# Kernel optimization log

Measured on AMD Instinct MI355X. Metric: run time of the kernel, lower is better.

Reference implementation:

```python
import jax, jax.numpy as jnp
import numpy as np

LONG, LAT = 256, 256
N = LONG * LAT
BATCH = 64
OUT_DIM = 16 * 16


def _build_coo():
    # Faithful reproduction of the torch init loops (vectorized):
    # identity diagonal + 8-neighbor stencil entries for interior rows,
    # each (x,y) pair added in BOTH (x,y) and (y,x) directions.
    # torch sparse matmul on the uncoalesced COO sums duplicate entries,
    # so shared interior edges effectively get weight 2 -- the .at[].add
    # scatter below reproduces exactly that summation semantics.
    diag = np.arange(N, dtype=np.int64)
    centers = np.arange(LAT + 1, (LONG - 1) * LAT - 1, dtype=np.int64)
    offs = np.array([-1, 1, LAT, -LAT, LAT - 1, LAT + 1, -LAT - 1, -LAT + 1], dtype=np.int64)
    neigh = (centers[:, None] + offs[None, :]).ravel()
    crep = np.repeat(centers, 8)
    rows = np.concatenate([diag, crep, neigh]).astype(np.int32)
    cols = np.concatenate([diag, neigh, crep]).astype(np.int32)
    vals = np.ones(rows.shape[0], dtype=np.float32)
    return rows, cols, vals


def setup_inputs() -> dict:
    key = jax.random.key(0)
    k1, k2, k3 = jax.random.split(key, 3)
    rows, cols, vals = _build_coo()
    x = jax.random.normal(k1, (BATCH, LONG, LAT), dtype=jnp.float32)
    W = jax.random.normal(k2, (OUT_DIM, N), dtype=jnp.float32) * 0.02  # lin1.weight
    b = jax.random.normal(k3, (OUT_DIM,), dtype=jnp.float32) * 0.02   # lin1.bias
    return {
        "x": x,
        "W": W,
        "b": b,
        "rows": jnp.asarray(rows),
        "cols": jnp.asarray(cols),
        "vals": jnp.asarray(vals),
    }


def reference(x, W, b, rows, cols, vals):
    B = x.shape[0]
    xf = x.reshape(B, -1)                      # [B, N]
    gathered = xf[:, cols] * vals               # [B, E]
    h1 = jnp.zeros((B, xf.shape[1]), xf.dtype).at[:, rows].add(gathered)  # A @ xf.T, transposed
    h2 = h1 @ W.T + b                           # dense linear
    return h2
```

## Files before the change

### kernel.cpp

```cpp
#include <hip/hip_runtime.h>
#include <hip/hip_bf16.h>


#define MB    64
#define NOUT  256
#define KDIM  65536
#define NTOT  (MB * KDIM)
#define KSP   256
#define NCH   (KDIM / KSP)
#define OTOT  (MB * NOUT)
#define LSTR  272

typedef __attribute__((ext_vector_type(8))) short bf16x8;
typedef __attribute__((ext_vector_type(8))) unsigned short ushort8v;
typedef __attribute__((ext_vector_type(4))) float f32x4;

__device__ __forceinline__ ushort f2bf(float f) {
    __hip_bfloat16 h = __float2bfloat16(f);
    return *reinterpret_cast<ushort*>(&h);
}
__device__ __forceinline__ float bf2f(ushort u) {
    return __uint_as_float((unsigned)u << 16);
}

__device__ __forceinline__ void stencil16v(const float* __restrict__ x, int g,
                                           ushort8v* o0, ushort8v* o1) {
    const int i8 = g & (KDIM - 1);
    union Span { float4 v[6]; float f[24]; };
    Span u, c, d;
    #pragma unroll
    for (int q = 0; q < 6; ++q) {
        int bu = g - 260 + 4 * q; if (bu < 0) bu = 0;
        int bc = g - 4   + 4 * q; if (bc < 0) bc = 0; if (bc > NTOT - 4) bc = NTOT - 4;
        int bd = g + 252 + 4 * q; if (bd > NTOT - 4) bd = NTOT - 4;
        u.v[q] = *(const float4*)(x + bu);
        c.v[q] = *(const float4*)(x + bc);
        d.v[q] = *(const float4*)(x + bd);
    }
    if (i8 >= 514 && i8 <= 65006) {
        #pragma unroll
        for (int e = 0; e < 16; ++e) {
            float nb = c.f[3 + e] + c.f[5 + e]
                     + u.f[3 + e] + u.f[4 + e] + u.f[5 + e]
                     + d.f[3 + e] + d.f[4 + e] + d.f[5 + e];
            const ushort o = f2bf(fmaf(2.0f, nb, c.f[4 + e]));
            if (e < 8) (*o0)[e] = o; else (*o1)[e - 8] = o;
        }
    } else {
        #pragma unroll
        for (int e = 0; e < 16; ++e) {
            const int ii = i8 + e;
            const float ci = ((unsigned)(ii - 257) <= (65278u - 257u)) ? 1.0f : 0.0f;
            float s = c.f[4 + e];
            const int   doff[8] = {-1, 1, -257, -256, -255, 255, 256, 257};
            const float* src[8] = {&c.f[3 + e], &c.f[5 + e],
                                   &u.f[3 + e], &u.f[4 + e], &u.f[5 + e],
                                   &d.f[3 + e], &d.f[4 + e], &d.f[5 + e]};
            #pragma unroll
            for (int t = 0; t < 8; ++t) {
                const int j = ii + doff[t];
                const float cj = ((unsigned)(j - 257) <= (65278u - 257u)) ? 1.0f : 0.0f;
                s = fmaf(ci + cj, *src[t], s);
            }
            const ushort o = f2bf(s);
            if (e < 8) (*o0)[e] = o; else (*o1)[e - 8] = o;
        }
    }
}

__global__ __launch_bounds__(1024, 4) void fused_sg(const float* __restrict__ x,
                                                    const float* __restrict__ W,
                                                    ushort* __restrict__ part) {
    __shared__ ushort hs[MB * LSTR];
    const int b  = blockIdx.x;
    const int kp = (b & 7) * 32 + (b >> 3);
    const int t  = threadIdx.x;

    {
        const int m = t >> 4;
        const int j = t & 15;
        const int g = m * KDIM + kp * KSP + j * 16;
        ushort8v o0, o1;
        stencil16v(x, g, &o0, &o1);
        *(ushort8v*)&hs[m * LSTR + j * 16]     = o0;
        *(ushort8v*)&hs[m * LSTR + j * 16 + 8] = o1;
    }
    __syncthreads();

    const int nt = t >> 6;
    const int l  = t & 63;
    const int lr = l & 15;
    const int lg = l >> 4;

    f32x4 acc0 = (f32x4){0.f,0.f,0.f,0.f}, acc1 = (f32x4){0.f,0.f,0.f,0.f};
    f32x4 acc2 = (f32x4){0.f,0.f,0.f,0.f}, acc3 = (f32x4){0.f,0.f,0.f,0.f};

    const float* wp = W + (size_t)(nt * 16 + lr) * KDIM + kp * KSP + lg * 8;

    #pragma unroll
    for (int ks = 0; ks < KSP / 32; ++ks) {
        float4 w0 = *(const float4*)(wp + ks * 32);
        float4 w1 = *(const float4*)(wp + ks * 32 + 4);
        union { ushort u[8]; bf16x8 v; } bb;
        bb.u[0] = f2bf(w0.x); bb.u[1] = f2bf(w0.y);
        bb.u[2] = f2bf(w0.z); bb.u[3] = f2bf(w0.w);
        bb.u[4] = f2bf(w1.x); bb.u[5] = f2bf(w1.y);
        bb.u[6] = f2bf(w1.z); bb.u[7] = f2bf(w1.w);
        bf16x8 af0 = *(const bf16x8*)&hs[(0 * 16 + lr) * LSTR + lg * 8 + ks * 32];
        bf16x8 af1 = *(const bf16x8*)&hs[(1 * 16 + lr) * LSTR + lg * 8 + ks * 32];
        bf16x8 af2 = *(const bf16x8*)&hs[(2 * 16 + lr) * LSTR + lg * 8 + ks * 32];
        bf16x8 af3 = *(const bf16x8*)&hs[(3 * 16 + lr) * LSTR + lg * 8 + ks * 32];
        acc0 = __builtin_amdgcn_mfma_f32_16x16x32_bf16(af0, bb.v, acc0, 0, 0, 0);
        acc1 = __builtin_amdgcn_mfma_f32_16x16x32_bf16(af1, bb.v, acc1, 0, 0, 0);
        acc2 = __builtin_amdgcn_mfma_f32_16x16x32_bf16(af2, bb.v, acc2, 0, 0, 0);
        acc3 = __builtin_amdgcn_mfma_f32_16x16x32_bf16(af3, bb.v, acc3, 0, 0, 0);
    }

    ushort* pb = part + (size_t)kp * OTOT + (size_t)(nt * 16 + lr) * MB;
    ushort4 s;
    s.x = f2bf(acc0[0]); s.y = f2bf(acc0[1]); s.z = f2bf(acc0[2]); s.w = f2bf(acc0[3]);
    *(ushort4*)(pb + 0 * 16 + lg * 4) = s;
    s.x = f2bf(acc1[0]); s.y = f2bf(acc1[1]); s.z = f2bf(acc1[2]); s.w = f2bf(acc1[3]);
    *(ushort4*)(pb + 1 * 16 + lg * 4) = s;
    s.x = f2bf(acc2[0]); s.y = f2bf(acc2[1]); s.z = f2bf(acc2[2]); s.w = f2bf(acc2[3]);
    *(ushort4*)(pb + 2 * 16 + lg * 4) = s;
    s.x = f2bf(acc3[0]); s.y = f2bf(acc3[1]); s.z = f2bf(acc3[2]); s.w = f2bf(acc3[3]);
    *(ushort4*)(pb + 3 * 16 + lg * 4) = s;
}

__global__ __launch_bounds__(256) void reduce_bf16(const ushort* __restrict__ part,
                                                   const float* __restrict__ bias,
                                                   float* __restrict__ out) {
    __shared__ float red[256];
    const int ol = threadIdx.x & 15;
    const int cg = threadIdx.x >> 4;
    const int o  = blockIdx.x * 16 + ol;
    const ushort* p = part + (size_t)cg * 16 * OTOT + o;
    float s0 = 0.f, s1 = 0.f, s2 = 0.f, s3 = 0.f;
    #pragma unroll
    for (int i = 0; i < 16; i += 4) {
        s0 += bf2f(p[(size_t)(i + 0) * OTOT]);
        s1 += bf2f(p[(size_t)(i + 1) * OTOT]);
        s2 += bf2f(p[(size_t)(i + 2) * OTOT]);
        s3 += bf2f(p[(size_t)(i + 3) * OTOT]);
    }
    red[threadIdx.x] = (s0 + s1) + (s2 + s3);
    __syncthreads();
    if (cg == 0) {
        float v = red[ol];
        #pragma unroll
        for (int jj = 1; jj < 16; ++jj) v += red[jj * 16 + ol];
        const int n = o >> 6, m = o & 63;
        out[m * NOUT + n] = v + bias[n];
    }
}

extern "C" void kernel_launch(void* const* d_in, const int* in_sizes, int n_in,
                              void* d_out, int out_size, void* d_ws, size_t ws_size,
                              hipStream_t stream) {
    const float* x    = (const float*)d_in[0];
    const float* W    = (const float*)d_in[1];
    const float* bias = (const float*)d_in[2];
    float* out = (float*)d_out;

    ushort* part = (ushort*)d_ws;

    fused_sg<<<NCH, 1024, 0, stream>>>(x, W, part);
    reduce_bf16<<<OTOT / 16, 256, 0, stream>>>(part, bias, out);
}
```

Baseline: 35.05 us.

## Use 2D 16x16 spatial tiles with shared-memory staged stencil halo

Each block now covers a 16x16 spatial tile instead of one 256-wide row strip. It first loads the tile plus a one-cell halo for all 64 batches into shared memory as bf16, then computes the 9-point stencil from shared memory. This is meant to stop each thread from re-reading three overlapping rows straight from global memory. The cost is a larger shared-memory footprint, which may lower occupancy, an extra sync, and W loads that are now strided across rows. The input is also rounded to bf16 before the stencil sums, which adds rounding error.

Result: no change. 35.69 us (+1.8%).

```diff
diff --git a/kernel.cpp b/kernel.cpp
--- a/kernel.cpp
+++ b/kernel.cpp
@@ -6,10 +6,10 @@
 #define NOUT  256
 #define KDIM  65536
 #define NTOT  (MB * KDIM)
-#define KSP   256
-#define NCH   (KDIM / KSP)
 #define OTOT  (MB * NOUT)
 #define LSTR  272
+#define XSM   432
+#define XSR   24
 
 typedef __attribute__((ext_vector_type(8))) short bf16x8;
 typedef __attribute__((ext_vector_type(8))) unsigned short ushort8v;
@@ -23,67 +23,82 @@
     return __uint_as_float((unsigned)u << 16);
 }
 
-__device__ __forceinline__ void stencil16v(const float* __restrict__ x, int g,
-                                           ushort8v* o0, ushort8v* o1) {
-    const int i8 = g & (KDIM - 1);
-    union Span { float4 v[6]; float f[24]; };
-    Span u, c, d;
-    #pragma unroll
-    for (int q = 0; q < 6; ++q) {
-        int bu = g - 260 + 4 * q; if (bu < 0) bu = 0;
-        int bc = g - 4   + 4 * q; if (bc < 0) bc = 0; if (bc > NTOT - 4) bc = NTOT - 4;
-        int bd = g + 252 + 4 * q; if (bd > NTOT - 4) bd = NTOT - 4;
-        u.v[q] = *(const float4*)(x + bu);
-        c.v[q] = *(const float4*)(x + bc);
-        d.v[q] = *(const float4*)(x + bd);
-    }
-    if (i8 >= 514 && i8 <= 65006) {
-        #pragma unroll
-        for (int e = 0; e < 16; ++e) {
-            float nb = c.f[3 + e] + c.f[5 + e]
-                     + u.f[3 + e] + u.f[4 + e] + u.f[5 + e]
-                     + d.f[3 + e] + d.f[4 + e] + d.f[5 + e];
-            const ushort o = f2bf(fmaf(2.0f, nb, c.f[4 + e]));
-            if (e < 8) (*o0)[e] = o; else (*o1)[e - 8] = o;
-        }
-    } else {
-        #pragma unroll
-        for (int e = 0; e < 16; ++e) {
-            const int ii = i8 + e;
-            const float ci = ((unsigned)(ii - 257) <= (65278u - 257u)) ? 1.0f : 0.0f;
-            float s = c.f[4 + e];
-            const int   doff[8] = {-1, 1, -257, -256, -255, 255, 256, 257};
-            const float* src[8] = {&c.f[3 + e], &c.f[5 + e],
-                                   &u.f[3 + e], &u.f[4 + e], &u.f[5 + e],
-                                   &d.f[3 + e], &d.f[4 + e], &d.f[5 + e]};
-            #pragma unroll
-            for (int t = 0; t < 8; ++t) {
-                const int j = ii + doff[t];
-                const float cj = ((unsigned)(j - 257) <= (65278u - 257u)) ? 1.0f : 0.0f;
-                s = fmaf(ci + cj, *src[t], s);
-            }
-            const ushort o = f2bf(s);
-            if (e < 8) (*o0)[e] = o; else (*o1)[e - 8] = o;
-        }
-    }
-}
-
 __global__ __launch_bounds__(1024, 4) void fused_sg(const float* __restrict__ x,
                                                     const float* __restrict__ W,
                                                     ushort* __restrict__ part) {
+    __shared__ ushort xs[MB * XSM];
     __shared__ ushort hs[MB * LSTR];
-    const int b  = blockIdx.x;
-    const int kp = (b & 7) * 32 + (b >> 3);
-    const int t  = threadIdx.x;
+    const int b   = blockIdx.x;
+    const int tid = (b & 7) * 32 + (b >> 3);
+    const int r0  = (tid >> 4) << 4;
+    const int c0  = (tid & 15) << 4;
+    const int t   = threadIdx.x;
+
+    #pragma unroll
+    for (int it = 0; it < 7; ++it) {
+        const int cid = t + it * 1024;
+        if (cid < 6912) {
+            const int m   = cid / 108;
+            const int rem = cid - m * 108;
+            const int rr  = rem / 6;
+            const int q   = rem - rr * 6;
+            int a = m * KDIM + (r0 + rr - 1) * 256 + (c0 - 4 + q * 4);
+            a = a < 0 ? 0 : (a > NTOT - 4 ? NTOT - 4 : a);
+            const float4 v = *(const float4*)(x + a);
+            ushort4 s;
+            s.x = f2bf(v.x); s.y = f2bf(v.y); s.z = f2bf(v.z); s.w = f2bf(v.w);
+            *(ushort4*)&xs[m * XSM + rr * XSR + q * 4] = s;
+        }
+    }
+    __syncthreads();
 
     {
-        const int m = t >> 4;
-        const int j = t & 15;
-        const int g = m * KDIM + kp * KSP + j * 16;
-        ushort8v o0, o1;
-        stencil16v(x, g, &o0, &o1);
-        *(ushort8v*)&hs[m * LSTR + j * 16]     = o0;
-        *(ushort8v*)&hs[m * LSTR + j * 16 + 8] = o1;
+        const int m2 = t >> 4;
+        const int rs = t & 15;
+        ushort8v rowv[3][3];
+        #pragma unroll
+        for (int r = 0; r < 3; ++r) {
+            const int base = m2 * XSM + (rs + r) * XSR;
+            rowv[r][0] = *(const ushort8v*)&xs[base];
+            rowv[r][1] = *(const ushort8v*)&xs[base + 8];
+            rowv[r][2] = *(const ushort8v*)&xs[base + 16];
+        }
+#define XE(R, C) bf2f((ushort)rowv[R][(C) >> 3][(C) & 7])
+        const int ibase = (r0 + rs) * 256 + c0;
+        ushort8v h0, h1v;
+        if (ibase >= 514 && ibase <= 65006) {
+            #pragma unroll
+            for (int cs = 0; cs < 16; ++cs) {
+                const float nb = XE(1, cs + 3) + XE(1, cs + 5)
+                               + XE(0, cs + 3) + XE(0, cs + 4) + XE(0, cs + 5)
+                               + XE(2, cs + 3) + XE(2, cs + 4) + XE(2, cs + 5);
+                const ushort o = f2bf(fmaf(2.0f, nb, XE(1, cs + 4)));
+                if (cs < 8) h0[cs] = o; else h1v[cs - 8] = o;
+            }
+        } else {
+            #pragma unroll
+            for (int cs = 0; cs < 16; ++cs) {
+                const int i = ibase + cs;
+                const float ci = ((unsigned)(i - 257) <= (65278u - 257u)) ? 1.0f : 0.0f;
+                float s = XE(1, cs + 4);
+                float v0 = XE(1, cs + 3), v1 = XE(1, cs + 5);
+                float v2 = XE(0, cs + 3), v3 = XE(0, cs + 4), v4 = XE(0, cs + 5);
+                float v5 = XE(2, cs + 3), v6 = XE(2, cs + 4), v7 = XE(2, cs + 5);
+                const int joff[8] = {-1, 1, -257, -256, -255, 255, 256, 257};
+                const float vals[8] = {v0, v1, v2, v3, v4, v5, v6, v7};
+                #pragma unroll
+                for (int e = 0; e < 8; ++e) {
+                    const int jf = i + joff[e];
+                    const float cj = ((unsigned)(jf - 257) <= (65278u - 257u)) ? 1.0f : 0.0f;
+                    s = fmaf(ci + cj, vals[e], s);
+                }
+                const ushort o = f2bf(s);
+                if (cs < 8) h0[cs] = o; else h1v[cs - 8] = o;
+            }
+        }
+#undef XE
+        *(ushort8v*)&hs[m2 * LSTR + rs * 16]     = h0;
+        *(ushort8v*)&hs[m2 * LSTR + rs * 16 + 8] = h1v;
     }
     __syncthreads();
 
@@ -95,12 +110,13 @@
     f32x4 acc0 = (f32x4){0.f,0.f,0.f,0.f}, acc1 = (f32x4){0.f,0.f,0.f,0.f};
     f32x4 acc2 = (f32x4){0.f,0.f,0.f,0.f}, acc3 = (f32x4){0.f,0.f,0.f,0.f};
 
-    const float* wp = W + (size_t)(nt * 16 + lr) * KDIM + kp * KSP + lg * 8;
+    const float* wb = W + (size_t)(nt * 16 + lr) * KDIM
+                        + (size_t)(r0 + (lg >> 1)) * 256 + c0 + (lg & 1) * 8;
 
     #pragma unroll
-    for (int ks = 0; ks < KSP / 32; ++ks) {
-        float4 w0 = *(const float4*)(wp + ks * 32);
-        float4 w1 = *(const float4*)(wp + ks * 32 + 4);
+    for (int ks = 0; ks < 8; ++ks) {
+        float4 w0 = *(const float4*)(wb + ks * 512);
+        float4 w1 = *(const float4*)(wb + ks * 512 + 4);
         union { ushort u[8]; bf16x8 v; } bb;
         bb.u[0] = f2bf(w0.x); bb.u[1] = f2bf(w0.y);
         bb.u[2] = f2bf(w0.z); bb.u[3] = f2bf(w0.w);
@@ -116,7 +132,7 @@
         acc3 = __builtin_amdgcn_mfma_f32_16x16x32_bf16(af3, bb.v, acc3, 0, 0, 0);
     }
 
-    ushort* pb = part + (size_t)kp * OTOT + (size_t)(nt * 16 + lr) * MB;
+    ushort* pb = part + (size_t)tid * OTOT + (size_t)(nt * 16 + lr) * MB;
     ushort4 s;
     s.x = f2bf(acc0[0]); s.y = f2bf(acc0[1]); s.z = f2bf(acc0[2]); s.w = f2bf(acc0[3]);
     *(ushort4*)(pb + 0 * 16 + lg * 4) = s;
@@ -165,6 +181,6 @@
 
     ushort* part = (ushort*)d_ws;
 
-    fused_sg<<<NCH, 1024, 0, stream>>>(x, W, part);
+    fused_sg<<<256, 1024, 0, stream>>>(x, W, part);
     reduce_bf16<<<OTOT / 16, 256, 0, stream>>>(part, bias, out);
 }
```
